# Kernel tuning notes

Hardware: AMD Instinct MI355X
Metric: run time of the kernel (lower is better)

## Reference

```python
import jax, jax.numpy as jnp
import numpy as np

N_NODES = 100000
N_EDGES = 1600000
D_IN = 128
D_HID = 128
D_OUT = 128


def setup_inputs() -> dict:
    key = jax.random.key(0)
    ks = jax.random.split(key, 8)
    x = jax.random.normal(ks[0], (N_NODES, D_IN), dtype=jnp.float32)
    edge_index = jax.random.randint(ks[1], (2, N_EDGES), 0, N_NODES, dtype=jnp.int64)
    # GraphConv layer 1: lin_rel (with bias) applied to aggregated messages, lin_root (no bias) to x
    s1 = 1.0 / np.sqrt(D_IN)
    W1_rel = jax.random.uniform(ks[2], (D_IN, D_HID), jnp.float32, -s1, s1)
    b1 = jax.random.uniform(ks[3], (D_HID,), jnp.float32, -s1, s1)
    W1_root = jax.random.uniform(ks[4], (D_IN, D_HID), jnp.float32, -s1, s1)
    s2 = 1.0 / np.sqrt(D_HID)
    W2_rel = jax.random.uniform(ks[5], (D_HID, D_OUT), jnp.float32, -s2, s2)
    b2 = jax.random.uniform(ks[6], (D_OUT,), jnp.float32, -s2, s2)
    W2_root = jax.random.uniform(ks[7], (D_HID, D_OUT), jnp.float32, -s2, s2)
    return {"x": x, "edge_index": edge_index, "W1_rel": W1_rel, "b1": b1,
            "W1_root": W1_root, "W2_rel": W2_rel, "b2": b2, "W2_root": W2_root}


def graph_conv(x, src, dst, W_rel, b, W_root, n_nodes):
    # PyG GraphConv (aggr='add'): out_i = W_rel @ sum_{j->i} x_j + b + W_root @ x_i
    msgs = jnp.take(x, src, axis=0)                       # [E, F] gather
    agg = jax.ops.segment_sum(msgs, dst, num_segments=n_nodes)  # [N, F] scatter-add
    return agg @ W_rel + b + x @ W_root


def reference(x, edge_index, W1_rel, b1, W1_root, W2_rel, b2, W2_root):
    src, dst = edge_index[0], edge_index[1]
    n = x.shape[0]
    h = graph_conv(x, src, dst, W1_rel, b1, W1_root, n)
    h = jax.nn.relu(h)
    out = graph_conv(h, src, dst, W2_rel, b2, W2_root, n)
    return out
```

## Files before the change

### kernel.cpp

```cpp
#include <hip/hip_runtime.h>

#define D 128
#define TILE_R 32
#define LDS_STRIDE 260
#define GBM 64
#define APAD 264

#define NB 512
#define NPB 256
#define EPB_A 2048

typedef __attribute__((ext_vector_type(8))) short bf16x8;
typedef __attribute__((ext_vector_type(4))) float f32x4;

static __device__ __forceinline__ ushort f2b(float f) {
    union { float f; uint u; } v; v.f = f;
    uint r = (v.u + 0x7FFFu + ((v.u >> 16) & 1u)) >> 16;
    return (ushort)r;
}
static __device__ __forceinline__ float blo(uint u) {
    union { uint u; float f; } v; v.u = u << 16; return v.f;
}
static __device__ __forceinline__ float bhi(uint u) {
    union { uint u; float f; } v; v.u = u & 0xFFFF0000u; return v.f;
}


__global__ __launch_bounds__(256) void bucket_count_kernel(
    const int* __restrict__ dst, int* __restrict__ bcnt, int nedges)
{
    __shared__ int h[NB];
    int t = threadIdx.x;
    for (int i = t; i < NB; i += 256) h[i] = 0;
    __syncthreads();
    int base = blockIdx.x * EPB_A;
    #pragma unroll
    for (int i = 0; i < 8; ++i) {
        int e = base + i * 256 + t;
        if (e < nedges) atomicAdd(&h[dst[e] >> 8], 1);
    }
    __syncthreads();
    for (int i = t; i < NB; i += 256) if (h[i]) atomicAdd(&bcnt[i], h[i]);
}

__global__ __launch_bounds__(512) void bucket_scan_kernel(
    const int* __restrict__ bcnt, int* __restrict__ bbase, int* __restrict__ bcur)
{
    __shared__ int sh[NB];
    int t = threadIdx.x;
    int v = bcnt[t];
    sh[t] = v; __syncthreads();
    int val = v;
    for (int off = 1; off < NB; off <<= 1) {
        int u = (t >= off) ? sh[t - off] : 0;
        __syncthreads();
        val += u; sh[t] = val; __syncthreads();
    }
    int excl = val - v;
    bbase[t] = excl;
    bcur[t] = excl;
}

__global__ __launch_bounds__(256) void bucket_scatter_kernel(
    const int* __restrict__ src, const int* __restrict__ dst,
    int* __restrict__ bcur, uint* __restrict__ ebuf, int nedges)
{
    __shared__ int h[NB];
    __shared__ int res[NB];
    int t = threadIdx.x;
    for (int i = t; i < NB; i += 256) h[i] = 0;
    __syncthreads();
    int base = blockIdx.x * EPB_A;
    int d[8], s[8], bkt[8];
    #pragma unroll
    for (int i = 0; i < 8; ++i) {
        int e = base + i * 256 + t;
        if (e < nedges) {
            d[i] = dst[e]; s[i] = src[e]; bkt[i] = d[i] >> 8;
            atomicAdd(&h[bkt[i]], 1);
        } else bkt[i] = -1;
    }
    __syncthreads();
    for (int i = t; i < NB; i += 256) {
        int c = h[i];
        res[i] = c ? atomicAdd(&bcur[i], c) : 0;
    }
    __syncthreads();
    #pragma unroll
    for (int i = 0; i < 8; ++i) {
        if (bkt[i] >= 0) {
            int pos = atomicAdd(&res[bkt[i]], 1);
            ebuf[pos] = ((uint)(d[i] & (NPB - 1)) << 17) | (uint)s[i];
        }
    }
}

__global__ __launch_bounds__(256) void csr_finalize_kernel(
    const uint* __restrict__ ebuf, const int* __restrict__ bbase,
    const int* __restrict__ bcnt, int* __restrict__ csr_src,
    int* __restrict__ ends, int n)
{
    __shared__ int cnt[NPB];
    __shared__ int cur[NPB];
    __shared__ int sh[NPB];
    int b = blockIdx.x, t = threadIdx.x;
    int ebase = bbase[b];
    int ecnt = bcnt[b];
    cnt[t] = 0;
    __syncthreads();
    for (int i = t; i < ecnt; i += 256)
        atomicAdd(&cnt[ebuf[ebase + i] >> 17], 1);
    __syncthreads();
    int v = cnt[t];
    sh[t] = v; __syncthreads();
    int val = v;
    for (int off = 1; off < 256; off <<= 1) {
        int u = (t >= off) ? sh[t - off] : 0;
        __syncthreads();
        val += u; sh[t] = val; __syncthreads();
    }
    int node = b * NPB + t;
    if (node < n) ends[node] = ebase + val;
    cur[t] = ebase + (val - v);
    __syncthreads();
    for (int i = t; i < ecnt; i += 256) {
        uint p = ebuf[ebase + i];
        int pos = atomicAdd(&cur[p >> 17], 1);
        csr_src[pos] = (int)(p & 0x1FFFFu);
    }
}


__global__ __launch_bounds__(256) void conv_f32_bf16_kernel(
    const float* __restrict__ in, ushort* __restrict__ out, int n8)
{
    int i = blockIdx.x * 256 + threadIdx.x;
    if (i >= n8) return;
    float4 a = reinterpret_cast<const float4*>(in)[i * 2];
    float4 b = reinterpret_cast<const float4*>(in)[i * 2 + 1];
    uint4 r;
    r.x = f2b(a.x) | ((uint)f2b(a.y) << 16);
    r.y = f2b(a.z) | ((uint)f2b(a.w) << 16);
    r.z = f2b(b.x) | ((uint)f2b(b.y) << 16);
    r.w = f2b(b.z) | ((uint)f2b(b.w) << 16);
    reinterpret_cast<uint4*>(out)[i] = r;
}

__global__ __launch_bounds__(256) void wt_kernel(
    const float* __restrict__ Wrel, const float* __restrict__ Wroot,
    ushort* __restrict__ Wt)
{
    int idx = blockIdx.x * 256 + threadIdx.x;
    int n = idx >> 8, k = idx & 255;
    float v = (k < 128) ? Wrel[(size_t)k * D + n] : Wroot[(size_t)(k - 128) * D + n];
    Wt[idx] = f2b(v);
}

__global__ __launch_bounds__(256) void gather_sum_bf16_kernel(
    const ushort* __restrict__ feat, const int* __restrict__ csr_src,
    const int* __restrict__ ends, ushort* __restrict__ aggb, int n)
{
    int node = blockIdx.x * 16 + (threadIdx.x >> 4);
    if (node >= n) return;
    int l = threadIdx.x & 15;
    int start = (node == 0) ? 0 : ends[node - 1];
    int end = ends[node];
    float a0=0,a1=0,a2=0,a3=0,a4=0,a5=0,a6=0,a7=0;
    for (int j = start; j < end; ++j) {
        int s = csr_src[j];
        uint4 v = reinterpret_cast<const uint4*>(feat + (size_t)s * D)[l];
        a0 += blo(v.x); a1 += bhi(v.x);
        a2 += blo(v.y); a3 += bhi(v.y);
        a4 += blo(v.z); a5 += bhi(v.z);
        a6 += blo(v.w); a7 += bhi(v.w);
    }
    uint4 r;
    r.x = f2b(a0) | ((uint)f2b(a1) << 16);
    r.y = f2b(a2) | ((uint)f2b(a3) << 16);
    r.z = f2b(a4) | ((uint)f2b(a5) << 16);
    r.w = f2b(a6) | ((uint)f2b(a7) << 16);
    reinterpret_cast<uint4*>(aggb + (size_t)node * D)[l] = r;
}

__global__ __launch_bounds__(256) void gemm_mfma_kernel(
    const ushort* __restrict__ A1, const ushort* A2,
    const ushort* __restrict__ Wt, const float* __restrict__ bias,
    float* outf, ushort* outb, int n, int mode)
{
    __shared__ ushort As[GBM * APAD];
    const int t = threadIdx.x;
    const int wave = t >> 6, lane = t & 63;
    const int base = blockIdx.x * GBM;

    #pragma unroll
    for (int m = 0; m < 8; ++m) {
        int q = t + m * 256;
        int r = q >> 5;
        int c = q & 31;
        int row = base + r;
        uint4 v = make_uint4(0, 0, 0, 0);
        if (row < n)
            v = (c < 16) ? reinterpret_cast<const uint4*>(A1 + (size_t)row * D)[c]
                         : reinterpret_cast<const uint4*>(A2 + (size_t)row * D)[c - 16];
        *reinterpret_cast<uint4*>(&As[r * APAD + c * 8]) = v;
    }

    const int bcol0 = wave * 32;
    bf16x8 Bfrag[2][8];
    #pragma unroll
    for (int nt = 0; nt < 2; ++nt)
        #pragma unroll
        for (int ks = 0; ks < 8; ++ks) {
            int ncol = bcol0 + nt * 16 + (lane & 15);
            int k = ks * 32 + (lane >> 4) * 8;
            Bfrag[nt][ks] = *reinterpret_cast<const bf16x8*>(Wt + (size_t)ncol * 256 + k);
        }

    __syncthreads();

    f32x4 acc[4][2];
    #pragma unroll
    for (int rt = 0; rt < 4; ++rt)
        #pragma unroll
        for (int nt = 0; nt < 2; ++nt) acc[rt][nt] = (f32x4){0.f, 0.f, 0.f, 0.f};

    #pragma unroll
    for (int ks = 0; ks < 8; ++ks) {
        bf16x8 a[4];
        #pragma unroll
        for (int rt = 0; rt < 4; ++rt) {
            int r = rt * 16 + (lane & 15);
            int k = ks * 32 + (lane >> 4) * 8;
            a[rt] = *reinterpret_cast<const bf16x8*>(&As[r * APAD + k]);
        }
        #pragma unroll
        for (int rt = 0; rt < 4; ++rt)
            #pragma unroll
            for (int nt = 0; nt < 2; ++nt)
                acc[rt][nt] = __builtin_amdgcn_mfma_f32_16x16x32_bf16(
                    a[rt], Bfrag[nt][ks], acc[rt][nt], 0, 0, 0);
    }

    #pragma unroll
    for (int rt = 0; rt < 4; ++rt)
        #pragma unroll
        for (int nt = 0; nt < 2; ++nt) {
            int col = bcol0 + nt * 16 + (lane & 15);
            float bv = bias[col];
            #pragma unroll
            for (int r = 0; r < 4; ++r) {
                int row = base + rt * 16 + (lane >> 4) * 4 + r;
                if (row >= n) continue;
                float v = acc[rt][nt][r] + bv;
                if (mode == 0) {
                    v = fmaxf(v, 0.f);
                    outb[(size_t)row * D + col] = f2b(v);
                } else {
                    outf[(size_t)row * D + col] = v;
                }
            }
        }
}


__global__ __launch_bounds__(256) void scatter_add_kernel(
    const float* __restrict__ feat, const int* __restrict__ src,
    const int* __restrict__ dst, float* agg, int nedges)
{
    int tid = blockIdx.x * 256 + threadIdx.x;
    int e = tid >> 5;
    if (e >= nedges) return;
    int l = tid & 31;
    int s = src[e];
    int d = dst[e];
    const float4 v = *reinterpret_cast<const float4*>(feat + (size_t)s * D + l * 4);
    float* o = agg + (size_t)d * D + l * 4;
    unsafeAtomicAdd(o + 0, v.x);
    unsafeAtomicAdd(o + 1, v.y);
    unsafeAtomicAdd(o + 2, v.z);
    unsafeAtomicAdd(o + 3, v.w);
}

__global__ __launch_bounds__(256) void gemm_fused_kernel(
    const float* __restrict__ A1, const float* A2,
    const float* __restrict__ Wrel, const float* __restrict__ Wroot,
    const float* __restrict__ bias, float* out, int n, int do_relu)
{
    __shared__ float Asf[TILE_R * LDS_STRIDE];
    const int t = threadIdx.x;
    const int base = blockIdx.x * TILE_R;

    #pragma unroll
    for (int m = 0; m < 8; ++m) {
        int q = t + m * 256;
        int r = q >> 6;
        int kk = (q & 63) << 2;
        int row = base + r;
        float4 v = make_float4(0.f, 0.f, 0.f, 0.f);
        if (row < n) {
            const float* p = (kk < 128) ? (A1 + (size_t)row * D + kk)
                                        : (A2 + (size_t)row * D + (kk - 128));
            v = *reinterpret_cast<const float4*>(p);
        }
        *reinterpret_cast<float4*>(&Asf[r * LDS_STRIDE + kk]) = v;
    }
    __syncthreads();

    const int rg = t >> 5;
    const int c0 = (t & 31) << 2;

    float acc[4][4];
    #pragma unroll
    for (int i = 0; i < 4; ++i)
        #pragma unroll
        for (int j = 0; j < 4; ++j) acc[i][j] = 0.f;

    const float* Wmats[2] = {Wrel, Wroot};
    #pragma unroll
    for (int half = 0; half < 2; ++half) {
        const float* W = Wmats[half];
        const int kb = half * 128;
        for (int k = 0; k < 128; k += 4) {
            float w[4][4];
            #pragma unroll
            for (int kk = 0; kk < 4; ++kk) {
                float4 wv = *reinterpret_cast<const float4*>(W + (size_t)(k + kk) * D + c0);
                w[kk][0] = wv.x; w[kk][1] = wv.y; w[kk][2] = wv.z; w[kk][3] = wv.w;
            }
            #pragma unroll
            for (int i = 0; i < 4; ++i) {
                float4 av = *reinterpret_cast<const float4*>(&Asf[(rg * 4 + i) * LDS_STRIDE + kb + k]);
                float a[4] = {av.x, av.y, av.z, av.w};
                #pragma unroll
                for (int kk = 0; kk < 4; ++kk)
                    #pragma unroll
                    for (int j = 0; j < 4; ++j)
                        acc[i][j] = fmaf(a[kk], w[kk][j], acc[i][j]);
            }
        }
    }

    float4 bv = *reinterpret_cast<const float4*>(bias + c0);
    float b[4] = {bv.x, bv.y, bv.z, bv.w};
    #pragma unroll
    for (int i = 0; i < 4; ++i) {
        int row = base + rg * 4 + i;
        if (row >= n) continue;
        float o[4];
        #pragma unroll
        for (int j = 0; j < 4; ++j) {
            float v = acc[i][j] + b[j];
            if (do_relu) v = fmaxf(v, 0.f);
            o[j] = v;
        }
        *reinterpret_cast<float4*>(out + (size_t)row * D + c0) =
            make_float4(o[0], o[1], o[2], o[3]);
    }
}

extern "C" void kernel_launch(void* const* d_in, const int* in_sizes, int n_in,
                              void* d_out, int out_size, void* d_ws, size_t ws_size,
                              hipStream_t stream) {
    const float* x       = (const float*)d_in[0];
    const int*   ei      = (const int*)d_in[1];
    const float* W1_rel  = (const float*)d_in[2];
    const float* b1      = (const float*)d_in[3];
    const float* W1_root = (const float*)d_in[4];
    const float* W2_rel  = (const float*)d_in[5];
    const float* b2      = (const float*)d_in[6];
    const float* W2_root = (const float*)d_in[7];
    float* out = (float*)d_out;

    const int E = in_sizes[1] / 2;
    const int N = in_sizes[0] / D;
    const int* src = ei;
    const int* dst = ei + E;

    size_t aggbB = ((size_t)N * D * 2 + 255) & ~(size_t)255;
    size_t xbB   = ((size_t)N * D * 2 + 255) & ~(size_t)255;
    size_t csrB  = ((size_t)E * 4 + 255) & ~(size_t)255;
    size_t endB  = ((size_t)(N + 1) * 4 + 255) & ~(size_t)255;
    size_t bktB  = ((size_t)(3 * NB + 8) * 4 + 255) & ~(size_t)255;
    size_t wtB   = (size_t)128 * 256 * 2;
    size_t need = aggbB + xbB + csrB + endB + bktB + 2 * wtB;

    bool pack_ok = (N <= 131072) && ((size_t)E * 4 <= aggbB);

    if (ws_size >= need && pack_ok) {
        char* w = (char*)d_ws;
        ushort* aggb    = (ushort*)w;            w += aggbB;
        ushort* xb      = (ushort*)w;            w += xbB;
        int*    csr_src = (int*)w;               w += csrB;
        int*    ends    = (int*)w;               w += endB;
        int*    bcnt    = (int*)w;
        int*    bbase   = bcnt + NB;
        int*    bcur    = bbase + NB;            w += bktB;
        ushort* Wt1     = (ushort*)w;            w += wtB;
        ushort* Wt2     = (ushort*)w;
        uint*   ebuf    = (uint*)aggb;

        const int aBlocks = (E + EPB_A - 1) / EPB_A;
        const int nbu = (N + NPB - 1) / NPB;

        hipMemsetAsync(bcnt, 0, NB * sizeof(int), stream);
        bucket_count_kernel<<<aBlocks, 256, 0, stream>>>(dst, bcnt, E);
        bucket_scan_kernel<<<1, NB, 0, stream>>>(bcnt, bbase, bcur);
        bucket_scatter_kernel<<<aBlocks, 256, 0, stream>>>(src, dst, bcur, ebuf, E);
        csr_finalize_kernel<<<nbu, 256, 0, stream>>>(ebuf, bbase, bcnt, csr_src, ends, N);

        int n8 = N * D / 8;
        conv_f32_bf16_kernel<<<(n8 + 255) / 256, 256, 0, stream>>>(x, xb, n8);
        wt_kernel<<<128, 256, 0, stream>>>(W1_rel, W1_root, Wt1);
        wt_kernel<<<128, 256, 0, stream>>>(W2_rel, W2_root, Wt2);

        int gatherBlocks = (N + 15) / 16;
        int gemmBlocks = (N + GBM - 1) / GBM;

        gather_sum_bf16_kernel<<<gatherBlocks, 256, 0, stream>>>(xb, csr_src, ends, aggb, N);
        gemm_mfma_kernel<<<gemmBlocks, 256, 0, stream>>>(aggb, xb, Wt1, b1, nullptr, xb, N, 0);
        gather_sum_bf16_kernel<<<gatherBlocks, 256, 0, stream>>>(xb, csr_src, ends, aggb, N);
        gemm_mfma_kernel<<<gemmBlocks, 256, 0, stream>>>(aggb, xb, Wt2, b2, out, nullptr, N, 1);
    } else {
        float* agg = (float*)d_ws;
        size_t aggBytes = (size_t)N * D * sizeof(float);
        int scatterBlocks = (E * 32 + 255) / 256;
        int gemmBlocks = (N + TILE_R - 1) / TILE_R;
        hipMemsetAsync(agg, 0, aggBytes, stream);
        scatter_add_kernel<<<scatterBlocks, 256, 0, stream>>>(x, src, dst, agg, E);
        gemm_fused_kernel<<<gemmBlocks, 256, 0, stream>>>(agg, x, W1_rel, W1_root, b1, out, N, 1);
        hipMemsetAsync(agg, 0, aggBytes, stream);
        scatter_add_kernel<<<scatterBlocks, 256, 0, stream>>>(out, src, dst, agg, E);
        gemm_fused_kernel<<<gemmBlocks, 256, 0, stream>>>(agg, out, W2_rel, W2_root, b2, out, N, 0);
    }
}
```

Before: 290.5 us.

## Fuse neighbor gather-sum into MFMA GEMM per 64-node tile

```diff
diff --git a/kernel.cpp b/kernel.cpp
--- a/kernel.cpp
+++ b/kernel.cpp
@@ -156,36 +156,11 @@
     Wt[idx] = f2b(v);
 }
 
-__global__ __launch_bounds__(256) void gather_sum_bf16_kernel(
+__global__ __launch_bounds__(256) void layer_fused_kernel(
     const ushort* __restrict__ feat, const int* __restrict__ csr_src,
-    const int* __restrict__ ends, ushort* __restrict__ aggb, int n)
-{
-    int node = blockIdx.x * 16 + (threadIdx.x >> 4);
-    if (node >= n) return;
-    int l = threadIdx.x & 15;
-    int start = (node == 0) ? 0 : ends[node - 1];
-    int end = ends[node];
-    float a0=0,a1=0,a2=0,a3=0,a4=0,a5=0,a6=0,a7=0;
-    for (int j = start; j < end; ++j) {
-        int s = csr_src[j];
-        uint4 v = reinterpret_cast<const uint4*>(feat + (size_t)s * D)[l];
-        a0 += blo(v.x); a1 += bhi(v.x);
-        a2 += blo(v.y); a3 += bhi(v.y);
-        a4 += blo(v.z); a5 += bhi(v.z);
-        a6 += blo(v.w); a7 += bhi(v.w);
-    }
-    uint4 r;
-    r.x = f2b(a0) | ((uint)f2b(a1) << 16);
-    r.y = f2b(a2) | ((uint)f2b(a3) << 16);
-    r.z = f2b(a4) | ((uint)f2b(a5) << 16);
-    r.w = f2b(a6) | ((uint)f2b(a7) << 16);
-    reinterpret_cast<uint4*>(aggb + (size_t)node * D)[l] = r;
-}
-
-__global__ __launch_bounds__(256) void gemm_mfma_kernel(
-    const ushort* __restrict__ A1, const ushort* A2,
-    const ushort* __restrict__ Wt, const float* __restrict__ bias,
-    float* outf, ushort* outb, int n, int mode)
+    const int* __restrict__ ends, const ushort* __restrict__ Wt,
+    const float* __restrict__ bias, float* outf, ushort* outb,
+    int n, int mode)
 {
     __shared__ ushort As[GBM * APAD];
     const int t = threadIdx.x;
@@ -193,59 +168,85 @@
     const int base = blockIdx.x * GBM;
 
     #pragma unroll
-    for (int m = 0; m < 8; ++m) {
+    for (int m = 0; m < 4; ++m) {
         int q = t + m * 256;
-        int r = q >> 5;
-        int c = q & 31;
+        int r = q >> 4, c = q & 15;
         int row = base + r;
         uint4 v = make_uint4(0, 0, 0, 0);
-        if (row < n)
-            v = (c < 16) ? reinterpret_cast<const uint4*>(A1 + (size_t)row * D)[c]
-                         : reinterpret_cast<const uint4*>(A2 + (size_t)row * D)[c - 16];
-        *reinterpret_cast<uint4*>(&As[r * APAD + c * 8]) = v;
-    }
+        if (row < n) v = reinterpret_cast<const uint4*>(feat + (size_t)row * D)[c];
+        *reinterpret_cast<uint4*>(&As[r * APAD + 128 + c * 8]) = v;
+    }
+
+    {
+        const int g = t >> 4, l = t & 15;
+        #pragma unroll 1
+        for (int sub = 0; sub < 4; ++sub) {
+            int r = g * 4 + sub;
+            int node = base + r;
+            float a0=0,a1=0,a2=0,a3=0,a4=0,a5=0,a6=0,a7=0;
+            float c0=0,c1=0,c2=0,c3=0,c4=0,c5=0,c6=0,c7=0;
+            if (node < n) {
+                int jb = (node == 0) ? 0 : ends[node - 1];
+                int je = ends[node];
+                int j = jb;
+                for (; j + 2 <= je; j += 2) {
+                    int s0 = csr_src[j], s1 = csr_src[j + 1];
+                    uint4 v0 = reinterpret_cast<const uint4*>(feat + (size_t)s0 * D)[l];
+                    uint4 v1 = reinterpret_cast<const uint4*>(feat + (size_t)s1 * D)[l];
+                    a0 += blo(v0.x); a1 += bhi(v0.x); a2 += blo(v0.y); a3 += bhi(v0.y);
+                    a4 += blo(v0.z); a5 += bhi(v0.z); a6 += blo(v0.w); a7 += bhi(v0.w);
+                    c0 += blo(v1.x); c1 += bhi(v1.x); c2 += blo(v1.y); c3 += bhi(v1.y);
+                    c4 += blo(v1.z); c5 += bhi(v1.z); c6 += blo(v1.w); c7 += bhi(v1.w);
+                }
+                if (j < je) {
+                    int s0 = csr_src[j];
+                    uint4 v0 = reinterpret_cast<const uint4*>(feat + (size_t)s0 * D)[l];
+                    a0 += blo(v0.x); a1 += bhi(v0.x); a2 += blo(v0.y); a3 += bhi(v0.y);
+                    a4 += blo(v0.z); a5 += bhi(v0.z); a6 += blo(v0.w); a7 += bhi(v0.w);
+                }
+            }
+            uint4 rp;
+            rp.x = f2b(a0 + c0) | ((uint)f2b(a1 + c1) << 16);
+            rp.y = f2b(a2 + c2) | ((uint)f2b(a3 + c3) << 16);
+            rp.z = f2b(a4 + c4) | ((uint)f2b(a5 + c5) << 16);
+            rp.w = f2b(a6 + c6) | ((uint)f2b(a7 + c7) << 16);
+            *reinterpret_cast<uint4*>(&As[r * APAD + l * 8]) = rp;
+        }
+    }
+    __syncthreads();
 
     const int bcol0 = wave * 32;
-    bf16x8 Bfrag[2][8];
-    #pragma unroll
-    for (int nt = 0; nt < 2; ++nt)
-        #pragma unroll
-        for (int ks = 0; ks < 8; ++ks) {
-            int ncol = bcol0 + nt * 16 + (lane & 15);
-            int k = ks * 32 + (lane >> 4) * 8;
-            Bfrag[nt][ks] = *reinterpret_cast<const bf16x8*>(Wt + (size_t)ncol * 256 + k);
-        }
-
-    __syncthreads();
-
+    const int l15 = lane & 15;
     f32x4 acc[4][2];
     #pragma unroll
     for (int rt = 0; rt < 4; ++rt)
         #pragma unroll
         for (int nt = 0; nt < 2; ++nt) acc[rt][nt] = (f32x4){0.f, 0.f, 0.f, 0.f};
 
-    #pragma unroll
+    #pragma unroll 1
     for (int ks = 0; ks < 8; ++ks) {
-        bf16x8 a[4];
-        #pragma unroll
-        for (int rt = 0; rt < 4; ++rt) {
-            int r = rt * 16 + (lane & 15);
-            int k = ks * 32 + (lane >> 4) * 8;
-            a[rt] = *reinterpret_cast<const bf16x8*>(&As[r * APAD + k]);
-        }
-        #pragma unroll
-        for (int rt = 0; rt < 4; ++rt)
-            #pragma unroll
-            for (int nt = 0; nt < 2; ++nt)
-                acc[rt][nt] = __builtin_amdgcn_mfma_f32_16x16x32_bf16(
-                    a[rt], Bfrag[nt][ks], acc[rt][nt], 0, 0, 0);
+        const int kk = ks * 32 + (lane >> 4) * 8;
+        bf16x8 a0_ = *reinterpret_cast<const bf16x8*>(&As[(l15 +  0) * APAD + kk]);
+        bf16x8 a1_ = *reinterpret_cast<const bf16x8*>(&As[(l15 + 16) * APAD + kk]);
+        bf16x8 a2_ = *reinterpret_cast<const bf16x8*>(&As[(l15 + 32) * APAD + kk]);
+        bf16x8 a3_ = *reinterpret_cast<const bf16x8*>(&As[(l15 + 48) * APAD + kk]);
+        bf16x8 b0_ = *reinterpret_cast<const bf16x8*>(Wt + (size_t)(bcol0 + l15) * 256 + kk);
+        bf16x8 b1_ = *reinterpret_cast<const bf16x8*>(Wt + (size_t)(bcol0 + 16 + l15) * 256 + kk);
+        acc[0][0] = __builtin_amdgcn_mfma_f32_16x16x32_bf16(a0_, b0_, acc[0][0], 0, 0, 0);
+        acc[0][1] = __builtin_amdgcn_mfma_f32_16x16x32_bf16(a0_, b1_, acc[0][1], 0, 0, 0);
+        acc[1][0] = __builtin_amdgcn_mfma_f32_16x16x32_bf16(a1_, b0_, acc[1][0], 0, 0, 0);
+        acc[1][1] = __builtin_amdgcn_mfma_f32_16x16x32_bf16(a1_, b1_, acc[1][1], 0, 0, 0);
+        acc[2][0] = __builtin_amdgcn_mfma_f32_16x16x32_bf16(a2_, b0_, acc[2][0], 0, 0, 0);
+        acc[2][1] = __builtin_amdgcn_mfma_f32_16x16x32_bf16(a2_, b1_, acc[2][1], 0, 0, 0);
+        acc[3][0] = __builtin_amdgcn_mfma_f32_16x16x32_bf16(a3_, b0_, acc[3][0], 0, 0, 0);
+        acc[3][1] = __builtin_amdgcn_mfma_f32_16x16x32_bf16(a3_, b1_, acc[3][1], 0, 0, 0);
     }
 
     #pragma unroll
     for (int rt = 0; rt < 4; ++rt)
         #pragma unroll
         for (int nt = 0; nt < 2; ++nt) {
-            int col = bcol0 + nt * 16 + (lane & 15);
+            int col = bcol0 + nt * 16 + l15;
             float bv = bias[col];
             #pragma unroll
             for (int r = 0; r < 4; ++r) {
@@ -376,19 +377,19 @@
     const int* src = ei;
     const int* dst = ei + E;
 
-    size_t aggbB = ((size_t)N * D * 2 + 255) & ~(size_t)255;
+    size_t hbB   = ((size_t)N * D * 2 + 255) & ~(size_t)255;
     size_t xbB   = ((size_t)N * D * 2 + 255) & ~(size_t)255;
     size_t csrB  = ((size_t)E * 4 + 255) & ~(size_t)255;
     size_t endB  = ((size_t)(N + 1) * 4 + 255) & ~(size_t)255;
     size_t bktB  = ((size_t)(3 * NB + 8) * 4 + 255) & ~(size_t)255;
     size_t wtB   = (size_t)128 * 256 * 2;
-    size_t need = aggbB + xbB + csrB + endB + bktB + 2 * wtB;
-
-    bool pack_ok = (N <= 131072) && ((size_t)E * 4 <= aggbB);
+    size_t need = hbB + xbB + csrB + endB + bktB + 2 * wtB;
+
+    bool pack_ok = (N <= 131072) && ((size_t)E * 4 <= hbB);
 
     if (ws_size >= need && pack_ok) {
         char* w = (char*)d_ws;
-        ushort* aggb    = (ushort*)w;            w += aggbB;
+        ushort* hb      = (ushort*)w;            w += hbB;
         ushort* xb      = (ushort*)w;            w += xbB;
         int*    csr_src = (int*)w;               w += csrB;
         int*    ends    = (int*)w;               w += endB;
@@ -397,7 +398,7 @@
         int*    bcur    = bbase + NB;            w += bktB;
         ushort* Wt1     = (ushort*)w;            w += wtB;
         ushort* Wt2     = (ushort*)w;
-        uint*   ebuf    = (uint*)aggb;
+        uint*   ebuf    = (uint*)hb;
 
         const int aBlocks = (E + EPB_A - 1) / EPB_A;
         const int nbu = (N + NPB - 1) / NPB;
@@ -413,13 +414,12 @@
         wt_kernel<<<128, 256, 0, stream>>>(W1_rel, W1_root, Wt1);
         wt_kernel<<<128, 256, 0, stream>>>(W2_rel, W2_root, Wt2);
 
-        int gatherBlocks = (N + 15) / 16;
-        int gemmBlocks = (N + GBM - 1) / GBM;
-
-        gather_sum_bf16_kernel<<<gatherBlocks, 256, 0, stream>>>(xb, csr_src, ends, aggb, N);
-        gemm_mfma_kernel<<<gemmBlocks, 256, 0, stream>>>(aggb, xb, Wt1, b1, nullptr, xb, N, 0);
-        gather_sum_bf16_kernel<<<gatherBlocks, 256, 0, stream>>>(xb, csr_src, ends, aggb, N);
-        gemm_mfma_kernel<<<gemmBlocks, 256, 0, stream>>>(aggb, xb, Wt2, b2, out, nullptr, N, 1);
+        int layerBlocks = (N + GBM - 1) / GBM;
+
+        layer_fused_kernel<<<layerBlocks, 256, 0, stream>>>(
+            xb, csr_src, ends, Wt1, b1, nullptr, hb, N, 0);
+        layer_fused_kernel<<<layerBlocks, 256, 0, stream>>>(
+            hb, csr_src, ends, Wt2, b2, out, nullptr, N, 1);
     } else {
         float* agg = (float*)d_ws;
         size_t aggBytes = (size_t)N * D * sizeof(float);
```

Measured after the change: 292.7 us. About the same (+0.7%).
